# Kernel tuning notes

Measured on AMD Instinct MI355X. Metric: run time of the kernel, lower is better.

Reference implementation:

```python
import jax, jax.numpy as jnp
import numpy as np

B, T, C, H = 128, 200, 171, 1024  # batch, timesteps, frame_dim, hidden


def setup_inputs() -> dict:
    key = jax.random.key(0)
    ks = jax.random.split(key, 16)
    s = 1.0 / np.sqrt(H)  # PyTorch default init range for LSTMCell/Linear

    def u(k, shape):
        return jax.random.uniform(k, shape, jnp.float32, -s, s)

    inp = {
        "seq": jax.random.normal(ks[0], (B, T, C), jnp.float32),
        # LSTMCell 1: input C -> hidden H
        "W_ih1": u(ks[1], (4 * H, C)), "W_hh1": u(ks[2], (4 * H, H)),
        "b_ih1": u(ks[3], (4 * H,)),   "b_hh1": u(ks[4], (4 * H,)),
        # LSTMCell 2: H -> H
        "W_ih2": u(ks[5], (4 * H, H)), "W_hh2": u(ks[6], (4 * H, H)),
        "b_ih2": u(ks[7], (4 * H,)),   "b_hh2": u(ks[8], (4 * H,)),
        # LSTMCell 3: H -> H
        "W_ih3": u(ks[9], (4 * H, H)), "W_hh3": u(ks[10], (4 * H, H)),
        "b_ih3": u(ks[11], (4 * H,)),  "b_hh3": u(ks[12], (4 * H,)),
        # decoder Linear: H -> C
        "W_dec": u(ks[13], (C, H)), "b_dec": u(ks[14], (C,)),
        "cond": 5, "gt": 5,
    }
    return inp


def _lstm_cell(x, h, c, W_ih, W_hh, b_ih, b_hh):
    # PyTorch LSTMCell gate order: i, f, g, o
    gates = x @ W_ih.T + b_ih + h @ W_hh.T + b_hh
    i, f, g, o = jnp.split(gates, 4, axis=-1)
    c_new = jax.nn.sigmoid(f) * c + jax.nn.sigmoid(i) * jnp.tanh(g)
    h_new = jax.nn.sigmoid(o) * jnp.tanh(c_new)
    return h_new, c_new


def reference(seq, W_ih1, W_hh1, b_ih1, b_hh1,
              W_ih2, W_hh2, b_ih2, b_hh2,
              W_ih3, W_hh3, b_ih3, b_hh3,
              W_dec, b_dec, cond, gt):
    Bb, Tt, Cc = seq.shape
    Hh = W_hh1.shape[1]
    # Static teacher-forcing pattern: gt ground-truth steps, then cond self-conditioned steps.
    pattern = jnp.asarray(np.array(([True] * gt + [False] * cond) * 100, dtype=bool)[:Tt])

    def step(carry, xs):
        h1, c1, h2, c2, h3, c3, xo = carry
        x_t, use_gt = xs
        x = jnp.where(use_gt, x_t, xo)
        h1, c1 = _lstm_cell(x, h1, c1, W_ih1, W_hh1, b_ih1, b_hh1)
        h2, c2 = _lstm_cell(h1, h2, c2, W_ih2, W_hh2, b_ih2, b_hh2)
        h3, c3 = _lstm_cell(h2, h3, c3, W_ih3, W_hh3, b_ih3, b_hh3)
        xo = h3 @ W_dec.T + b_dec
        return (h1, c1, h2, c2, h3, c3, xo), xo

    z = jnp.zeros((Bb, Hh), seq.dtype)
    init = (z, z, z, z, z, z, jnp.zeros((Bb, Cc), seq.dtype))
    _, out = jax.lax.scan(step, init, (seq.transpose(1, 0, 2), pattern))
    return out.transpose(1, 0, 2)  # [B, T, C]
```

## Files before the change

kernel.cpp:

```cpp
#include <hip/hip_runtime.h>

#define TT 200
#define BB 128
#define CC 171
#define HH 1024
#define XPAD 192
#define FOURH 4096

typedef __attribute__((ext_vector_type(8))) short short8;
typedef __attribute__((ext_vector_type(4))) float f32x4;

__device__ __forceinline__ unsigned short f2bf(float f) {
  unsigned int u = __float_as_uint(f);
  u += 0x7fff + ((u >> 16) & 1);
  return (unsigned short)(u >> 16);
}
__device__ __forceinline__ float sigmoidf_(float x) { return 1.f / (1.f + __expf(-x)); }

__device__ __forceinline__ int4 ld_coh16(const void* p) {
  int4 r;
  asm volatile("global_load_dwordx4 %0, %1, off sc0 sc1" : "=v"(r) : "v"(p));
  return r;
}
__device__ __forceinline__ void st_coh2(void* p, unsigned int v) {
  asm volatile("global_store_short %0, %1, off sc0 sc1" :: "v"(p), "v"(v) : "memory");
}
__device__ __forceinline__ void drain_vm() {
  asm volatile("s_waitcnt vmcnt(0)" ::: "memory");
}

__device__ __forceinline__ void gridbar(int* bar, int wg, int tid, int epoch) {
  drain_vm();
  __syncthreads();
  if (tid == 0) {
    int g = wg & 7;
    if (__hip_atomic_fetch_add(&bar[g * 32], 1, __ATOMIC_RELAXED, __HIP_MEMORY_SCOPE_AGENT) == 31) {
      if (__hip_atomic_fetch_add(&bar[512], 1, __ATOMIC_RELAXED, __HIP_MEMORY_SCOPE_AGENT) == 7) {
        __hip_atomic_store(&bar[512], 0, __ATOMIC_RELAXED, __HIP_MEMORY_SCOPE_AGENT);
        __hip_atomic_store(&bar[544], epoch, __ATOMIC_RELAXED, __HIP_MEMORY_SCOPE_AGENT);
      } else {
        while (__hip_atomic_load(&bar[544], __ATOMIC_RELAXED, __HIP_MEMORY_SCOPE_AGENT) < epoch)
          __builtin_amdgcn_s_sleep(1);
      }
      __hip_atomic_store(&bar[g * 32], 0, __ATOMIC_RELAXED, __HIP_MEMORY_SCOPE_AGENT);
      __hip_atomic_store(&bar[(8 + g) * 32], epoch, __ATOMIC_RELAXED, __HIP_MEMORY_SCOPE_AGENT);
    } else {
      while (__hip_atomic_load(&bar[(8 + g) * 32], __ATOMIC_RELAXED, __HIP_MEMORY_SCOPE_AGENT) < epoch)
        __builtin_amdgcn_s_sleep(1);
    }
  }
  asm volatile("" ::: "memory");
  __syncthreads();
}

template<int NKT1, int NKTTOT>
__device__ __forceinline__ void lstm_phase(
    const unsigned short* __restrict__ A1, int sA1,
    const unsigned short* __restrict__ A2, int sA2,
    const unsigned short* __restrict__ W, int sW,
    const float* __restrict__ bias,
    float& creg, unsigned short* __restrict__ Hout,
    char* smem, int m0, int n0, int ntile, int tid)
{
  constexpr int BASE = NKTTOT / 4;
  constexpr int REM = NKTTOT % 4;
  constexpr int MAXKT = BASE + (REM ? 1 : 0);

  const int wave = tid >> 6, lane = tid & 63;
  const int grp = wave >> 2, gw = wave & 3;
  const int lrow = lane >> 3, lj = lane & 7;
  const int fl = lane & 15, fh = lane >> 4;

  const int kt0 = grp * BASE + min(grp, REM);
  const int ktn = BASE + (grp < REM ? 1 : 0);

  char* Ar = smem + grp * 32768;
  const int row = gw * 8 + lrow;
  int4 areg[MAXKT];
#pragma unroll
  for (int i = 0; i < MAXKT; ++i) {
    if (i < ktn) {
      int kt = kt0 + i;
      const unsigned short* src; int col;
      if (kt < NKT1) { src = A1 + (size_t)(m0 + row) * sA1; col = kt * 64; }
      else           { src = A2 + (size_t)(m0 + row) * sA2; col = (kt - NKT1) * 64; }
      areg[i] = ld_coh16(src + col + ((lj ^ (row & 7)) << 3));
    }
  }
  drain_vm();
#pragma unroll
  for (int i = 0; i < MAXKT; ++i)
    if (i < ktn) *(int4*)(Ar + i * 4096 + row * 128 + lj * 16) = areg[i];
  __syncthreads();

  f32x4 acc0 = {0.f, 0.f, 0.f, 0.f}, acc1 = {0.f, 0.f, 0.f, 0.f};
  const unsigned short* Wrow = W + (size_t)(n0 + gw * 16 + fl) * sW + kt0 * 64 + fh * 8;
  const int swz = (fl & 7) << 4;
#pragma unroll
  for (int i = 0; i < MAXKT; ++i) {
    if (i < ktn) {
#pragma unroll
      for (int kk = 0; kk < 2; ++kk) {
        short8 b0 = *(const short8*)(Wrow + i * 64 + kk * 32);
        int colb = kk * 64 + fh * 16;
        short8 a0 = *(const short8*)(Ar + i * 4096 + fl * 128 + (colb ^ swz));
        short8 a1 = *(const short8*)(Ar + i * 4096 + (16 + fl) * 128 + (colb ^ swz));
        acc0 = __builtin_amdgcn_mfma_f32_16x16x32_bf16(a0, b0, acc0, 0, 0, 0);
        acc1 = __builtin_amdgcn_mfma_f32_16x16x32_bf16(a1, b0, acc1, 0, 0, 0);
      }
    }
  }

  __syncthreads();
  float* ex = (float*)smem;
#pragma unroll
  for (int r = 0; r < 4; ++r) {
    ex[((grp * 4 + gw) * 32 + fh * 4 + r) * 16 + fl] = acc0[r];
    ex[((grp * 4 + gw) * 32 + 16 + fh * 4 + r) * 16 + fl] = acc1[r];
  }
  __syncthreads();
  if (tid < 512) {
    int urow = tid >> 4, uu = tid & 15;
    float g4[4];
#pragma unroll
    for (int gg = 0; gg < 4; ++gg) {
      float s = ex[(gg * 32 + urow) * 16 + uu] + ex[((4 + gg) * 32 + urow) * 16 + uu]
              + ex[((8 + gg) * 32 + urow) * 16 + uu] + ex[((12 + gg) * 32 + urow) * 16 + uu];
      g4[gg] = s + bias[n0 + gg * 16 + uu];
    }
    float cn = sigmoidf_(g4[1]) * creg + sigmoidf_(g4[0]) * tanhf(g4[2]);
    creg = cn;
    st_coh2(Hout + (size_t)(m0 + urow) * HH + ntile * 16 + uu,
            (unsigned int)f2bf(sigmoidf_(g4[3]) * tanhf(cn)));
  }
}

__device__ __forceinline__ void dec_phase(
    const unsigned short* __restrict__ H3in, const unsigned short* __restrict__ Wd,
    const float* __restrict__ bd, float* __restrict__ out,
    const float* __restrict__ seq, unsigned short* __restrict__ X,
    int gt, int cond, int t, char* smem, int wg, int tid)
{
  if (wg >= 44) return;
  const int wave = tid >> 6, lane = tid & 63;
  const int lrow = lane >> 3, lj = lane & 7;
  const int fl = lane & 15, fh = lane >> 4;
  const int ntile = wg % 11, mtile = wg / 11;
  const int m0 = mtile * 32, n0 = ntile * 16;

  char* Dr = smem + wave * 4096;
  int4 r4[4];
#pragma unroll
  for (int j = 0; j < 4; ++j) {
    int row = j * 8 + lrow;
    r4[j] = ld_coh16(H3in + (size_t)(m0 + row) * HH + wave * 64 + ((lj ^ (row & 7)) << 3));
  }
  drain_vm();
#pragma unroll
  for (int j = 0; j < 4; ++j) {
    int row = j * 8 + lrow;
    *(int4*)(Dr + row * 128 + lj * 16) = r4[j];
  }
  __syncthreads();

  f32x4 acc0 = {0.f, 0.f, 0.f, 0.f}, acc1 = {0.f, 0.f, 0.f, 0.f};
  const unsigned short* Wrow = Wd + (size_t)(n0 + fl) * HH + wave * 64 + fh * 8;
  const int swz = (fl & 7) << 4;
#pragma unroll
  for (int kk = 0; kk < 2; ++kk) {
    short8 b0 = *(const short8*)(Wrow + kk * 32);
    int colb = kk * 64 + fh * 16;
    short8 a0 = *(const short8*)(Dr + fl * 128 + (colb ^ swz));
    short8 a1 = *(const short8*)(Dr + (16 + fl) * 128 + (colb ^ swz));
    acc0 = __builtin_amdgcn_mfma_f32_16x16x32_bf16(a0, b0, acc0, 0, 0, 0);
    acc1 = __builtin_amdgcn_mfma_f32_16x16x32_bf16(a1, b0, acc1, 0, 0, 0);
  }

  float* pex = (float*)(smem + 65536);
#pragma unroll
  for (int r = 0; r < 4; ++r) {
    pex[(wave * 32 + fh * 4 + r) * 16 + fl] = acc0[r];
    pex[(wave * 32 + 16 + fh * 4 + r) * 16 + fl] = acc1[r];
  }
  __syncthreads();
  if (tid < 512) {
    int row = tid >> 4, uu = tid & 15;
    int c = n0 + uu;
    if (c < CC) {
      float s = 0.f;
#pragma unroll
      for (int v = 0; v < 16; ++v) s += pex[(v * 32 + row) * 16 + uu];
      float val = s + bd[c];
      int batch = m0 + row;
      out[(size_t)batch * (TT * CC) + (size_t)t * CC + c] = val;
      if (t + 1 < TT) {
        int per = gt + cond;
        bool ug = (per > 0) ? (((t + 1) % per) < gt) : false;
        float xv = ug ? seq[(size_t)batch * (TT * CC) + (size_t)(t + 1) * CC + c] : val;
        st_coh2(X + batch * XPAD + c, (unsigned int)f2bf(xv));
      }
    }
  }
}

__global__ __launch_bounds__(1024, 4) void persistent_lstm(
    const unsigned short* __restrict__ W1, const unsigned short* __restrict__ W2,
    const unsigned short* __restrict__ W3, const unsigned short* __restrict__ Wd,
    const float* __restrict__ B1, const float* __restrict__ B2,
    const float* __restrict__ B3, const float* __restrict__ Bd,
    unsigned short* __restrict__ Hb, unsigned short* __restrict__ X,
    const float* __restrict__ seq, float* __restrict__ out,
    const int* __restrict__ gtp, const int* __restrict__ condp, int* __restrict__ bar)
{
  __shared__ char smem[131072];
  const int wg = blockIdx.x, tid = threadIdx.x;
  const int xg = wg & 7, sl = wg >> 3;
  const int ntile = xg * 8 + (sl >> 2);
  const int m0 = (sl & 3) * 32;
  const int n0 = ntile * 64;
  const int gt = *gtp, cond = *condp;

  unsigned short* H1[2] = { Hb + 0 * BB * HH, Hb + 1 * BB * HH };
  unsigned short* H2[2] = { Hb + 2 * BB * HH, Hb + 3 * BB * HH };
  unsigned short* H3[2] = { Hb + 4 * BB * HH, Hb + 5 * BB * HH };

  float c1 = 0.f, c2 = 0.f, c3 = 0.f;

  int epoch = 0;
  for (int t = 0; t < TT; ++t) {
    int p = t & 1;
    lstm_phase<3, 19>(X, XPAD, H1[p], HH, W1, 1216, B1, c1, H1[1 - p], smem, m0, n0, ntile, tid);
    gridbar(bar, wg, tid, ++epoch);
    lstm_phase<16, 32>(H1[1 - p], HH, H2[p], HH, W2, 2048, B2, c2, H2[1 - p], smem, m0, n0, ntile, tid);
    gridbar(bar, wg, tid, ++epoch);
    lstm_phase<16, 32>(H2[1 - p], HH, H3[p], HH, W3, 2048, B3, c3, H3[1 - p], smem, m0, n0, ntile, tid);
    gridbar(bar, wg, tid, ++epoch);
    dec_phase(H3[1 - p], Wd, Bd, out, seq, X, gt, cond, t, smem, wg, tid);
    gridbar(bar, wg, tid, ++epoch);
  }
}

__device__ __forceinline__ int perm_orig_row(int np) {
  return ((np >> 4) & 3) * HH + ((np >> 6) << 4) + (np & 15);
}

__global__ void conv_w1(const float* __restrict__ Wih, const float* __restrict__ Whh,
                        unsigned short* __restrict__ dst) {
  int k = blockIdx.x * 256 + threadIdx.x;
  int np = blockIdx.y;
  if (k >= 1216) return;
  int n = perm_orig_row(np);
  float v;
  if (k < XPAD) v = (k < CC) ? Wih[(size_t)n * CC + k] : 0.f;
  else          v = Whh[(size_t)n * HH + (k - XPAD)];
  dst[(size_t)np * 1216 + k] = f2bf(v);
}

__global__ void conv_w23(const float* __restrict__ Wih, const float* __restrict__ Whh,
                         unsigned short* __restrict__ dst) {
  int k = blockIdx.x * 256 + threadIdx.x;
  int np = blockIdx.y;
  int n = perm_orig_row(np);
  float v = (k < HH) ? Wih[(size_t)n * HH + k] : Whh[(size_t)n * HH + (k - HH)];
  dst[(size_t)np * 2048 + k] = f2bf(v);
}

__global__ void conv_wd(const float* __restrict__ Wsrc, unsigned short* __restrict__ dst) {
  int k = blockIdx.x * 256 + threadIdx.x;
  int row = blockIdx.y;
  float v = (row < CC) ? Wsrc[(size_t)row * HH + k] : 0.f;
  dst[(size_t)row * HH + k] = f2bf(v);
}

__global__ void conv_bias(const float* bi1, const float* bh1, const float* bi2, const float* bh2,
                          const float* bi3, const float* bh3, const float* bdec,
                          float* o1, float* o2, float* o3, float* od) {
  int idx = blockIdx.x * 256 + threadIdx.x;
  if (idx < 3 * FOURH) {
    int l = idx >> 12; int np = idx & 4095;
    int n = perm_orig_row(np);
    const float* bi = (l == 0) ? bi1 : ((l == 1) ? bi2 : bi3);
    const float* bh = (l == 0) ? bh1 : ((l == 1) ? bh2 : bh3);
    float* o = (l == 0) ? o1 : ((l == 1) ? o2 : o3);
    o[np] = bi[n] + bh[n];
  } else {
    int c2 = idx - 3 * FOURH;
    if (c2 < 176) od[c2] = (c2 < CC) ? bdec[c2] : 0.f;
  }
}

__global__ void init_state(unsigned short* __restrict__ Hall,
                           unsigned short* __restrict__ X, const float* __restrict__ seq,
                           const int* __restrict__ gtp, int* __restrict__ bar) {
  int idx = blockIdx.x * blockDim.x + threadIdx.x;
  if (idx < 3 * 2 * BB * HH) Hall[idx] = 0;
  if (idx < BB * XPAD) {
    int b = idx / XPAD, cc = idx % XPAD;
    float v = 0.f;
    if (cc < CC && (*gtp) > 0) v = seq[(size_t)b * TT * CC + cc];
    X[idx] = f2bf(v);
  }
  if (idx < 1024) bar[idx] = 0;
}

extern "C" void kernel_launch(void* const* d_in, const int* in_sizes, int n_in,
                              void* d_out, int out_size, void* d_ws, size_t ws_size,
                              hipStream_t stream)
{
  const float* seq   = (const float*)d_in[0];
  const float* W_ih1 = (const float*)d_in[1];
  const float* W_hh1 = (const float*)d_in[2];
  const float* b_ih1 = (const float*)d_in[3];
  const float* b_hh1 = (const float*)d_in[4];
  const float* W_ih2 = (const float*)d_in[5];
  const float* W_hh2 = (const float*)d_in[6];
  const float* b_ih2 = (const float*)d_in[7];
  const float* b_hh2 = (const float*)d_in[8];
  const float* W_ih3 = (const float*)d_in[9];
  const float* W_hh3 = (const float*)d_in[10];
  const float* b_ih3 = (const float*)d_in[11];
  const float* b_hh3 = (const float*)d_in[12];
  const float* W_dec = (const float*)d_in[13];
  const float* b_dec = (const float*)d_in[14];
  const int* condp   = (const int*)d_in[15];
  const int* gtp     = (const int*)d_in[16];
  float* out = (float*)d_out;
  char* ws = (char*)d_ws;

  if (ws_size < 47272960) return;

  unsigned short* W1 = (unsigned short*)(ws + 0);
  unsigned short* W2 = (unsigned short*)(ws + 9961472);
  unsigned short* W3 = (unsigned short*)(ws + 26738688);
  unsigned short* Wd = (unsigned short*)(ws + 43515904);
  float* B1 = (float*)(ws + 43876352);
  float* B2 = (float*)(ws + 43941888);
  float* B3 = (float*)(ws + 44007424);
  float* Bd = (float*)(ws + 44072960);
  unsigned short* Hbase = (unsigned short*)(ws + 44073984);
  unsigned short* X = (unsigned short*)(ws + 47219712);
  int* bar = (int*)(ws + 47268864);

  conv_w1 <<<dim3(5, 4096), 256, 0, stream>>>(W_ih1, W_hh1, W1);
  conv_w23<<<dim3(8, 4096), 256, 0, stream>>>(W_ih2, W_hh2, W2);
  conv_w23<<<dim3(8, 4096), 256, 0, stream>>>(W_ih3, W_hh3, W3);
  conv_wd <<<dim3(4, 176),  256, 0, stream>>>(W_dec, Wd);
  conv_bias<<<dim3(49), 256, 0, stream>>>(b_ih1, b_hh1, b_ih2, b_hh2, b_ih3, b_hh3, b_dec,
                                          B1, B2, B3, Bd);
  init_state<<<dim3(3072), 256, 0, stream>>>(Hbase, X, seq, gtp, bar);

  persistent_lstm<<<dim3(256), dim3(1024), 0, stream>>>(
      W1, W2, W3, Wd, B1, B2, B3, Bd, Hbase, X, seq, out, gtp, condp, bar);
}
```

Measured before the change: 7.685 ms.

## Fold decoder into layer-1 input weights and drop per-step decoder barrier

On self-conditioned steps, layer 1 now uses a precomputed fused weight W_ih1·W_dec (plus a folded bias) applied to h3 directly, so it no longer waits on the decoder output. The decoder output is computed off the critical path by a subset of workgroups, overlapped with the next step's layer-1 phase. This removes one grid barrier per timestep. Ground-truth steps read seq in fp32 and convert inline. The barrier is also reworked to use monotonic counters with no resets. The fused weight is rounded to bf16 after the product, which changes numerics slightly, and layer 1 does more MFMA work on self-conditioned steps (K=1024 instead of 192).

```diff
diff --git a/kernel.cpp b/kernel.cpp
--- a/kernel.cpp
+++ b/kernel.cpp
@@ -4,8 +4,6 @@
 #define BB 128
 #define CC 171
 #define HH 1024
-#define XPAD 192
-#define FOURH 4096
 
 typedef __attribute__((ext_vector_type(8))) short short8;
 typedef __attribute__((ext_vector_type(4))) float f32x4;
@@ -34,30 +32,28 @@
   __syncthreads();
   if (tid == 0) {
     int g = wg & 7;
-    if (__hip_atomic_fetch_add(&bar[g * 32], 1, __ATOMIC_RELAXED, __HIP_MEMORY_SCOPE_AGENT) == 31) {
-      if (__hip_atomic_fetch_add(&bar[512], 1, __ATOMIC_RELAXED, __HIP_MEMORY_SCOPE_AGENT) == 7) {
-        __hip_atomic_store(&bar[512], 0, __ATOMIC_RELAXED, __HIP_MEMORY_SCOPE_AGENT);
-        __hip_atomic_store(&bar[544], epoch, __ATOMIC_RELAXED, __HIP_MEMORY_SCOPE_AGENT);
-      } else {
-        while (__hip_atomic_load(&bar[544], __ATOMIC_RELAXED, __HIP_MEMORY_SCOPE_AGENT) < epoch)
-          __builtin_amdgcn_s_sleep(1);
+    int o = __hip_atomic_fetch_add(&bar[g * 32], 1, __ATOMIC_RELAXED, __HIP_MEMORY_SCOPE_AGENT);
+    if (o == epoch * 32 - 1) {
+      int m = __hip_atomic_fetch_add(&bar[960], 1, __ATOMIC_RELAXED, __HIP_MEMORY_SCOPE_AGENT);
+      if (m == epoch * 8 - 1) {
+#pragma unroll
+        for (int i = 0; i < 8; ++i)
+          __hip_atomic_store(&bar[(16 + i) * 32], epoch, __ATOMIC_RELAXED, __HIP_MEMORY_SCOPE_AGENT);
       }
-      __hip_atomic_store(&bar[g * 32], 0, __ATOMIC_RELAXED, __HIP_MEMORY_SCOPE_AGENT);
-      __hip_atomic_store(&bar[(8 + g) * 32], epoch, __ATOMIC_RELAXED, __HIP_MEMORY_SCOPE_AGENT);
-    } else {
-      while (__hip_atomic_load(&bar[(8 + g) * 32], __ATOMIC_RELAXED, __HIP_MEMORY_SCOPE_AGENT) < epoch)
-        __builtin_amdgcn_s_sleep(1);
-    }
+    }
+    while (__hip_atomic_load(&bar[(16 + g) * 32], __ATOMIC_RELAXED, __HIP_MEMORY_SCOPE_AGENT) < epoch)
+      __builtin_amdgcn_s_sleep(1);
   }
   asm volatile("" ::: "memory");
   __syncthreads();
 }
 
-template<int NKT1, int NKTTOT>
+template<int NKT1, int NKTTOT, bool A1SEQ>
 __device__ __forceinline__ void lstm_phase(
-    const unsigned short* __restrict__ A1, int sA1,
+    const void* A1v, int sA1,
     const unsigned short* __restrict__ A2, int sA2,
-    const unsigned short* __restrict__ W, int sW,
+    const unsigned short* __restrict__ Wa, int sWa,
+    const unsigned short* __restrict__ Wb, int sWb,
     const float* __restrict__ bias,
     float& creg, unsigned short* __restrict__ Hout,
     char* smem, int m0, int n0, int ntile, int tid)
@@ -81,10 +77,26 @@
   for (int i = 0; i < MAXKT; ++i) {
     if (i < ktn) {
       int kt = kt0 + i;
-      const unsigned short* src; int col;
-      if (kt < NKT1) { src = A1 + (size_t)(m0 + row) * sA1; col = kt * 64; }
-      else           { src = A2 + (size_t)(m0 + row) * sA2; col = (kt - NKT1) * 64; }
-      areg[i] = ld_coh16(src + col + ((lj ^ (row & 7)) << 3));
+      if (kt < NKT1) {
+        if constexpr (A1SEQ) {
+          const float* srow = (const float*)A1v + (size_t)(m0 + row) * sA1;
+          int c0 = kt * 64 + ((lj ^ (row & 7)) << 3);
+          unsigned int w[4];
+#pragma unroll
+          for (int j = 0; j < 4; ++j) {
+            int ca = c0 + 2 * j, cb = c0 + 2 * j + 1;
+            float va = (ca < CC) ? srow[ca] : 0.f;
+            float vb = (cb < CC) ? srow[cb] : 0.f;
+            w[j] = (unsigned int)f2bf(va) | ((unsigned int)f2bf(vb) << 16);
+          }
+          areg[i] = make_int4(w[0], w[1], w[2], w[3]);
+        } else {
+          const unsigned short* srow = (const unsigned short*)A1v + (size_t)(m0 + row) * sA1;
+          areg[i] = ld_coh16(srow + kt * 64 + ((lj ^ (row & 7)) << 3));
+        }
+      } else {
+        areg[i] = ld_coh16(A2 + (size_t)(m0 + row) * sA2 + (kt - NKT1) * 64 + ((lj ^ (row & 7)) << 3));
+      }
     }
   }
   drain_vm();
@@ -94,14 +106,18 @@
   __syncthreads();
 
   f32x4 acc0 = {0.f, 0.f, 0.f, 0.f}, acc1 = {0.f, 0.f, 0.f, 0.f};
-  const unsigned short* Wrow = W + (size_t)(n0 + gw * 16 + fl) * sW + kt0 * 64 + fh * 8;
+  const int wrowi = n0 + gw * 16 + fl;
   const int swz = (fl & 7) << 4;
 #pragma unroll
   for (int i = 0; i < MAXKT; ++i) {
     if (i < ktn) {
+      int kt = kt0 + i;
+      const unsigned short* wr = (kt < NKT1)
+          ? Wa + (size_t)wrowi * sWa + kt * 64 + fh * 8
+          : Wb + (size_t)wrowi * sWb + (kt - NKT1) * 64 + fh * 8;
 #pragma unroll
       for (int kk = 0; kk < 2; ++kk) {
-        short8 b0 = *(const short8*)(Wrow + i * 64 + kk * 32);
+        short8 b0 = *(const short8*)(wr + kk * 32);
         int colb = kk * 64 + fh * 16;
         short8 a0 = *(const short8*)(Ar + i * 4096 + fl * 128 + (colb ^ swz));
         short8 a1 = *(const short8*)(Ar + i * 4096 + (16 + fl) * 128 + (colb ^ swz));
@@ -135,20 +151,18 @@
   }
 }
 
-__device__ __forceinline__ void dec_phase(
+__device__ __forceinline__ void dec_out(
     const unsigned short* __restrict__ H3in, const unsigned short* __restrict__ Wd,
     const float* __restrict__ bd, float* __restrict__ out,
-    const float* __restrict__ seq, unsigned short* __restrict__ X,
-    int gt, int cond, int t, char* smem, int wg, int tid)
+    int t, char* smem, int d, int tid)
 {
-  if (wg >= 44) return;
   const int wave = tid >> 6, lane = tid & 63;
   const int lrow = lane >> 3, lj = lane & 7;
   const int fl = lane & 15, fh = lane >> 4;
-  const int ntile = wg % 11, mtile = wg / 11;
+  const int ntile = d % 11, mtile = d / 11;
   const int m0 = mtile * 32, n0 = ntile * 16;
 
-  char* Dr = smem + wave * 4096;
+  char* Dr = smem + 65536 + wave * 4096;
   int4 r4[4];
 #pragma unroll
   for (int j = 0; j < 4; ++j) {
@@ -161,7 +175,6 @@
     int row = j * 8 + lrow;
     *(int4*)(Dr + row * 128 + lj * 16) = r4[j];
   }
-  __syncthreads();
 
   f32x4 acc0 = {0.f, 0.f, 0.f, 0.f}, acc1 = {0.f, 0.f, 0.f, 0.f};
   const unsigned short* Wrow = Wd + (size_t)(n0 + fl) * HH + wave * 64 + fh * 8;
@@ -176,7 +189,7 @@
     acc1 = __builtin_amdgcn_mfma_f32_16x16x32_bf16(a1, b0, acc1, 0, 0, 0);
   }
 
-  float* pex = (float*)(smem + 65536);
+  float* pex = (float*)(smem + 32768);
 #pragma unroll
   for (int r = 0; r < 4; ++r) {
     pex[(wave * 32 + fh * 4 + r) * 16 + fl] = acc0[r];
@@ -190,26 +203,18 @@
       float s = 0.f;
 #pragma unroll
       for (int v = 0; v < 16; ++v) s += pex[(v * 32 + row) * 16 + uu];
-      float val = s + bd[c];
-      int batch = m0 + row;
-      out[(size_t)batch * (TT * CC) + (size_t)t * CC + c] = val;
-      if (t + 1 < TT) {
-        int per = gt + cond;
-        bool ug = (per > 0) ? (((t + 1) % per) < gt) : false;
-        float xv = ug ? seq[(size_t)batch * (TT * CC) + (size_t)(t + 1) * CC + c] : val;
-        st_coh2(X + batch * XPAD + c, (unsigned int)f2bf(xv));
-      }
-    }
-  }
-}
-
-__global__ __launch_bounds__(1024, 4) void persistent_lstm(
-    const unsigned short* __restrict__ W1, const unsigned short* __restrict__ W2,
+      out[(size_t)(m0 + row) * (TT * CC) + (size_t)t * CC + c] = s + bd[c];
+    }
+  }
+}
+
+__global__ __launch_bounds__(1024, 1) void persistent_lstm(
+    const unsigned short* __restrict__ Wih1p, const unsigned short* __restrict__ Whh1,
+    const unsigned short* __restrict__ Wf, const unsigned short* __restrict__ W2,
     const unsigned short* __restrict__ W3, const unsigned short* __restrict__ Wd,
-    const float* __restrict__ B1, const float* __restrict__ B2,
-    const float* __restrict__ B3, const float* __restrict__ Bd,
-    unsigned short* __restrict__ Hb, unsigned short* __restrict__ X,
-    const float* __restrict__ seq, float* __restrict__ out,
+    const float* __restrict__ B1gt, const float* __restrict__ B1sc,
+    const float* __restrict__ B2, const float* __restrict__ B3, const float* __restrict__ Bd,
+    unsigned short* __restrict__ Hb, const float* __restrict__ seq, float* __restrict__ out,
     const int* __restrict__ gtp, const int* __restrict__ condp, int* __restrict__ bar)
 {
   __shared__ char smem[131072];
@@ -219,41 +224,53 @@
   const int m0 = (sl & 3) * 32;
   const int n0 = ntile * 64;
   const int gt = *gtp, cond = *condp;
+  const int per = gt + cond;
+
+  int decid = -1;
+  if (sl >= 26) { int d = xg * 6 + (sl - 26); if (d < 44) decid = d; }
 
   unsigned short* H1[2] = { Hb + 0 * BB * HH, Hb + 1 * BB * HH };
   unsigned short* H2[2] = { Hb + 2 * BB * HH, Hb + 3 * BB * HH };
   unsigned short* H3[2] = { Hb + 4 * BB * HH, Hb + 5 * BB * HH };
 
   float c1 = 0.f, c2 = 0.f, c3 = 0.f;
-
-  int epoch = 0;
+  int e = 0, tm = 0;
   for (int t = 0; t < TT; ++t) {
     int p = t & 1;
-    lstm_phase<3, 19>(X, XPAD, H1[p], HH, W1, 1216, B1, c1, H1[1 - p], smem, m0, n0, ntile, tid);
-    gridbar(bar, wg, tid, ++epoch);
-    lstm_phase<16, 32>(H1[1 - p], HH, H2[p], HH, W2, 2048, B2, c2, H2[1 - p], smem, m0, n0, ntile, tid);
-    gridbar(bar, wg, tid, ++epoch);
-    lstm_phase<16, 32>(H2[1 - p], HH, H3[p], HH, W3, 2048, B3, c3, H3[1 - p], smem, m0, n0, ntile, tid);
-    gridbar(bar, wg, tid, ++epoch);
-    dec_phase(H3[1 - p], Wd, Bd, out, seq, X, gt, cond, t, smem, wg, tid);
-    gridbar(bar, wg, tid, ++epoch);
-  }
+    bool gts = (per > 0) ? (tm < gt) : true;
+    if (gts)
+      lstm_phase<3, 19, true>(seq + (size_t)t * CC, TT * CC, H1[p], HH,
+                              Wih1p, 192, Whh1, HH, B1gt, c1, H1[1 - p], smem, m0, n0, ntile, tid);
+    else
+      lstm_phase<16, 32, false>(H3[p], HH, H1[p], HH,
+                                Wf, HH, Whh1, HH, B1sc, c1, H1[1 - p], smem, m0, n0, ntile, tid);
+    if (t > 0 && decid >= 0) dec_out(H3[p], Wd, Bd, out, t - 1, smem, decid, tid);
+    gridbar(bar, wg, tid, ++e);
+    lstm_phase<16, 32, false>(H1[1 - p], HH, H2[p], HH,
+                              W2, 2048, W2 + 1024, 2048, B2, c2, H2[1 - p], smem, m0, n0, ntile, tid);
+    gridbar(bar, wg, tid, ++e);
+    lstm_phase<16, 32, false>(H2[1 - p], HH, H3[p], HH,
+                              W3, 2048, W3 + 1024, 2048, B3, c3, H3[1 - p], smem, m0, n0, ntile, tid);
+    gridbar(bar, wg, tid, ++e);
+    if (++tm == per) tm = 0;
+  }
+  if (decid >= 0) dec_out(H3[0], Wd, Bd, out, TT - 1, smem, decid, tid);
 }
 
 __device__ __forceinline__ int perm_orig_row(int np) {
   return ((np >> 4) & 3) * HH + ((np >> 6) << 4) + (np & 15);
 }
 
-__global__ void conv_w1(const float* __restrict__ Wih, const float* __restrict__ Whh,
-                        unsigned short* __restrict__ dst) {
-  int k = blockIdx.x * 256 + threadIdx.x;
-  int np = blockIdx.y;
-  if (k >= 1216) return;
+__global__ void conv_wih1p(const float* __restrict__ Wih, unsigned short* __restrict__ dst) {
+  int np = blockIdx.x, k = threadIdx.x;
   int n = perm_orig_row(np);
-  float v;
-  if (k < XPAD) v = (k < CC) ? Wih[(size_t)n * CC + k] : 0.f;
-  else          v = Whh[(size_t)n * HH + (k - XPAD)];
-  dst[(size_t)np * 1216 + k] = f2bf(v);
+  dst[(size_t)np * 192 + k] = f2bf((k < CC) ? Wih[(size_t)n * CC + k] : 0.f);
+}
+
+__global__ void conv_whh1(const float* __restrict__ Whh, unsigned short* __restrict__ dst) {
+  int np = blockIdx.y, k = blockIdx.x * 256 + threadIdx.x;
+  int n = perm_orig_row(np);
+  dst[(size_t)np * HH + k] = f2bf(Whh[(size_t)n * HH + k]);
 }
 
 __global__ void conv_w23(const float* __restrict__ Wih, const float* __restrict__ Whh,
@@ -268,38 +285,47 @@
 __global__ void conv_wd(const float* __restrict__ Wsrc, unsigned short* __restrict__ dst) {
   int k = blockIdx.x * 256 + threadIdx.x;
   int row = blockIdx.y;
-  float v = (row < CC) ? Wsrc[(size_t)row * HH + k] : 0.f;
-  dst[(size_t)row * HH + k] = f2bf(v);
-}
-
-__global__ void conv_bias(const float* bi1, const float* bh1, const float* bi2, const float* bh2,
-                          const float* bi3, const float* bh3, const float* bdec,
-                          float* o1, float* o2, float* o3, float* od) {
+  dst[(size_t)row * HH + k] = f2bf((row < CC) ? Wsrc[(size_t)row * HH + k] : 0.f);
+}
+
+__global__ void wf_gemm(const float* __restrict__ Wih1, const float* __restrict__ Wdec,
+                        unsigned short* __restrict__ Wfo) {
+  int j = blockIdx.x * 256 + threadIdx.x;
+  int np = blockIdx.y;
+  int n = perm_orig_row(np);
+  const float* wr = Wih1 + (size_t)n * CC;
+  float acc = 0.f;
+  for (int c = 0; c < CC; ++c) acc = fmaf(wr[c], Wdec[(size_t)c * HH + j], acc);
+  Wfo[(size_t)np * HH + j] = f2bf(acc);
+}
+
+__global__ void bias_all(const float* bi1, const float* bh1, const float* Wih1, const float* bdec,
+                         const float* bi2, const float* bh2, const float* bi3, const float* bh3,
+                         float* o1gt, float* o1sc, float* o2, float* o3, float* od) {
   int idx = blockIdx.x * 256 + threadIdx.x;
-  if (idx < 3 * FOURH) {
-    int l = idx >> 12; int np = idx & 4095;
-    int n = perm_orig_row(np);
-    const float* bi = (l == 0) ? bi1 : ((l == 1) ? bi2 : bi3);
-    const float* bh = (l == 0) ? bh1 : ((l == 1) ? bh2 : bh3);
-    float* o = (l == 0) ? o1 : ((l == 1) ? o2 : o3);
-    o[np] = bi[n] + bh[n];
-  } else {
-    int c2 = idx - 3 * FOURH;
-    if (c2 < 176) od[c2] = (c2 < CC) ? bdec[c2] : 0.f;
-  }
-}
-
-__global__ void init_state(unsigned short* __restrict__ Hall,
-                           unsigned short* __restrict__ X, const float* __restrict__ seq,
-                           const int* __restrict__ gtp, int* __restrict__ bar) {
+  if (idx < 4096) {
+    int n = perm_orig_row(idx);
+    float b = bi1[n] + bh1[n];
+    o1gt[idx] = b;
+    const float* wr = Wih1 + (size_t)n * CC;
+    float acc = 0.f;
+    for (int c = 0; c < CC; ++c) acc = fmaf(wr[c], bdec[c], acc);
+    o1sc[idx] = b + acc;
+  } else if (idx < 8192) {
+    int np = idx - 4096; int n = perm_orig_row(np);
+    o2[np] = bi2[n] + bh2[n];
+  } else if (idx < 12288) {
+    int np = idx - 8192; int n = perm_orig_row(np);
+    o3[np] = bi3[n] + bh3[n];
+  } else if (idx < 12464) {
+    int c2 = idx - 12288;
+    od[c2] = (c2 < CC) ? bdec[c2] : 0.f;
+  }
+}
+
+__global__ void init_state(unsigned short* __restrict__ Hall, int* __restrict__ bar) {
   int idx = blockIdx.x * blockDim.x + threadIdx.x;
-  if (idx < 3 * 2 * BB * HH) Hall[idx] = 0;
-  if (idx < BB * XPAD) {
-    int b = idx / XPAD, cc = idx % XPAD;
-    float v = 0.f;
-    if (cc < CC && (*gtp) > 0) v = seq[(size_t)b * TT * CC + cc];
-    X[idx] = f2bf(v);
-  }
+  if (idx < 6 * BB * HH) Hall[idx] = 0;
   if (idx < 1024) bar[idx] = 0;
 }
 
@@ -327,28 +353,34 @@
   float* out = (float*)d_out;
   char* ws = (char*)d_ws;
 
-  if (ws_size < 47272960) return;
-
-  unsigned short* W1 = (unsigned short*)(ws + 0);
-  unsigned short* W2 = (unsigned short*)(ws + 9961472);
-  unsigned short* W3 = (unsigned short*)(ws + 26738688);
-  unsigned short* Wd = (unsigned short*)(ws + 43515904);
-  float* B1 = (float*)(ws + 43876352);
-  float* B2 = (float*)(ws + 43941888);
-  float* B3 = (float*)(ws + 44007424);
-  float* Bd = (float*)(ws + 44072960);
-  unsigned short* Hbase = (unsigned short*)(ws + 44073984);
-  unsigned short* X = (unsigned short*)(ws + 47219712);
-  int* bar = (int*)(ws + 47268864);
-
-  conv_w1 <<<dim3(5, 4096), 256, 0, stream>>>(W_ih1, W_hh1, W1);
-  conv_w23<<<dim3(8, 4096), 256, 0, stream>>>(W_ih2, W_hh2, W2);
-  conv_w23<<<dim3(8, 4096), 256, 0, stream>>>(W_ih3, W_hh3, W3);
-  conv_wd <<<dim3(4, 176),  256, 0, stream>>>(W_dec, Wd);
-  conv_bias<<<dim3(49), 256, 0, stream>>>(b_ih1, b_hh1, b_ih2, b_hh2, b_ih3, b_hh3, b_dec,
-                                          B1, B2, B3, Bd);
-  init_state<<<dim3(3072), 256, 0, stream>>>(Hbase, X, seq, gtp, bar);
+  if (ws_size < 53908480) return;
+
+  unsigned short* Wih1p = (unsigned short*)(ws + 0);
+  unsigned short* Whh1  = (unsigned short*)(ws + 1572864);
+  unsigned short* Wf    = (unsigned short*)(ws + 9961472);
+  unsigned short* W2    = (unsigned short*)(ws + 18350080);
+  unsigned short* W3    = (unsigned short*)(ws + 35127296);
+  unsigned short* Wd    = (unsigned short*)(ws + 51904512);
+  float* B1gt = (float*)(ws + 52264960);
+  float* B1sc = (float*)(ws + 52281344);
+  float* B2   = (float*)(ws + 52297728);
+  float* B3   = (float*)(ws + 52314112);
+  float* Bd   = (float*)(ws + 52330496);
+  unsigned short* Hbase = (unsigned short*)(ws + 52331520);
+  int* bar = (int*)(ws + 53904384);
+
+  conv_wih1p<<<dim3(4096),    192, 0, stream>>>(W_ih1, Wih1p);
+  conv_whh1 <<<dim3(4, 4096), 256, 0, stream>>>(W_hh1, Whh1);
+  wf_gemm   <<<dim3(4, 4096), 256, 0, stream>>>(W_ih1, W_dec, Wf);
+  conv_w23  <<<dim3(8, 4096), 256, 0, stream>>>(W_ih2, W_hh2, W2);
+  conv_w23  <<<dim3(8, 4096), 256, 0, stream>>>(W_ih3, W_hh3, W3);
+  conv_wd   <<<dim3(4, 176),  256, 0, stream>>>(W_dec, Wd);
+  bias_all  <<<dim3(49),      256, 0, stream>>>(b_ih1, b_hh1, W_ih1, b_dec,
+                                                b_ih2, b_hh2, b_ih3, b_hh3,
+                                                B1gt, B1sc, B2, B3, Bd);
+  init_state<<<dim3(3072),    256, 0, stream>>>(Hbase, bar);
 
   persistent_lstm<<<dim3(256), dim3(1024), 0, stream>>>(
-      W1, W2, W3, Wd, B1, B2, B3, Bd, Hbase, X, seq, out, gtp, condp, bar);
-}
+      Wih1p, Whh1, Wf, W2, W3, Wd, B1gt, B1sc, B2, B3, Bd,
+      Hbase, seq, out, gtp, condp, bar);
+}
```

After: 8.043 ms. 4.7% more time.
